# Performance work log

Hardware: AMD Instinct MI355X
Metric: run time of the kernel (lower is better)

## Reference

```python
import jax, jax.numpy as jnp
import numpy as np

H = 8          # num heads
DK = 64        # d_model // H
D_MODEL = 512
WIN = 256


def setup_inputs() -> dict:
    key = jax.random.key(0)
    ks = jax.random.split(key, 12)
    B, S = 2, 2048
    mk = lambda k, shape, s=1.0: jax.random.normal(k, shape, dtype=jnp.float32) * s
    inp = {
        "query": mk(ks[0], (B, S, D_MODEL)),
        "key_in": mk(ks[1], (B, S, D_MODEL)),
        "value": mk(ks[2], (B, S, D_MODEL)),
        # nn.Linear(d_model, d_model) weights (out,in) and biases, x4
        "Wq": mk(ks[3], (D_MODEL, D_MODEL), 0.02), "bq": jnp.zeros((D_MODEL,), jnp.float32),
        "Wk": mk(ks[4], (D_MODEL, D_MODEL), 0.02), "bk": jnp.zeros((D_MODEL,), jnp.float32),
        "Wv": mk(ks[5], (D_MODEL, D_MODEL), 0.02), "bv": jnp.zeros((D_MODEL,), jnp.float32),
        "Wo": mk(ks[6], (D_MODEL, D_MODEL), 0.02), "bo": jnp.zeros((D_MODEL,), jnp.float32),
    }
    return inp


def reference(query, key_in, value, Wq, bq, Wk, bk, Wv, bv, Wo, bo):
    B, S, D = query.shape
    scale = np.float32(1.0 / np.sqrt(DK))

    def proj(x, W, b):
        # (B,S,D) -> (B,H,S,DK)
        return (x @ W.T + b).reshape(B, S, H, DK).transpose(0, 2, 1, 3)

    q = proj(query, Wq, bq)
    k = proj(key_in, Wk, bk)
    v = proj(value, Wv, bv)

    # Faithful to naive_masked_matmul: full (B,H,S,S) scores, with entries
    # OUTSIDE the sliding window left at exactly 0.0 (NOT -inf) before softmax.
    scores = jnp.einsum('bhid,bhjd->bhij', q, k) * scale
    idx = jnp.arange(S)
    band = jnp.abs(idx[:, None] - idx[None, :]) <= (WIN // 2)  # (S,S) bool
    scores = jnp.where(band, scores, jnp.float32(0.0))

    p_attn = jax.nn.softmax(scores, axis=-1)
    x = jnp.einsum('bhij,bhjd->bhid', p_attn, v)          # (B,H,S,DK)
    x = x.transpose(0, 2, 1, 3).reshape(B, S, D)          # (B,S,D)
    return x @ Wo.T + bo
```

## Files before the change

kernel.cpp:

```cpp
#include <hip/hip_runtime.h>
#include <hip/hip_bf16.h>

#define SS 2048
#define DD 512
#define HWIN 128

typedef __bf16 bf16x8 __attribute__((ext_vector_type(8)));
typedef unsigned short u16x8 __attribute__((ext_vector_type(8)));
typedef float f32x4 __attribute__((ext_vector_type(4)));

__device__ __forceinline__ unsigned short f2bf(float x) {
    unsigned u = __builtin_bit_cast(unsigned, x);
    return (unsigned short)((u + 0x7fffu + ((u >> 16) & 1u)) >> 16);
}
__device__ __forceinline__ float bf2f(unsigned short s) {
    unsigned u = ((unsigned)s) << 16;
    return __builtin_bit_cast(float, u);
}
__device__ __forceinline__ void split_bf(float x, unsigned short& h, unsigned short& l) {
    h = f2bf(x);
    l = f2bf(x - bf2f(h));
}
__device__ __forceinline__ void split8(float4 f0, float4 f1, u16x8& h, u16x8& l) {
    const float vals[8] = {f0.x, f0.y, f0.z, f0.w, f1.x, f1.y, f1.z, f1.w};
    #pragma unroll
    for (int i = 0; i < 8; ++i) {
        unsigned short hh, ll;
        split_bf(vals[i], hh, ll);
        h[i] = hh;
        l[i] = ll;
    }
}
__device__ __forceinline__ f32x4 mfma16(u16x8 a, u16x8 b, f32x4 c) {
    return __builtin_amdgcn_mfma_f32_16x16x32_bf16(
        __builtin_bit_cast(bf16x8, a), __builtin_bit_cast(bf16x8, b), c, 0, 0, 0);
}
__device__ __forceinline__ void gload16(const unsigned short* g, unsigned short* l) {
    __builtin_amdgcn_global_load_lds(
        (const __attribute__((address_space(1))) unsigned int*)g,
        (__attribute__((address_space(3))) unsigned int*)l, 16, 0, 0);
}

__global__ __launch_bounds__(256) void castAll(
    const float* __restrict__ q, const float* __restrict__ k, const float* __restrict__ v,
    const float* __restrict__ wq, const float* __restrict__ wk,
    const float* __restrict__ wv, const float* __restrict__ wo,
    unsigned short* __restrict__ QAh, unsigned short* __restrict__ KAh,
    unsigned short* __restrict__ AVp,
    unsigned short* __restrict__ WQh, unsigned short* __restrict__ WKh,
    unsigned short* __restrict__ WVp, unsigned short* __restrict__ WoP)
{
    const size_t e0 = ((size_t)blockIdx.x * 256 + threadIdx.x) * 8;
    const float* src; size_t off; unsigned short* dsth; bool paired;
    if      (e0 < 2097152) { src = q; off = e0;           dsth = QAh + off;     paired = false; }
    else if (e0 < 4194304) { src = k; off = e0 - 2097152; dsth = KAh + off;     paired = false; }
    else if (e0 < 6291456) { src = v; off = e0 - 4194304; dsth = AVp + 2 * off; paired = true;  }
    else {
        const size_t e = e0 - 6291456;
        if      (e < 262144) { src = wq; off = e;          dsth = WQh + off;                paired = false; }
        else if (e < 524288) { src = wk; off = e - 262144; dsth = WKh + off;                paired = false; }
        else if (e < 786432) { src = wv; off = e - 524288; dsth = WVp + 2 * (e - 524288);   paired = true;  }
        else                 { src = wo; off = e - 786432; dsth = WoP + 2 * (e - 786432);   paired = true;  }
    }
    u16x8 h, l;
    split8(*(const float4*)(src + off), *(const float4*)(src + off + 4), h, l);
    *(u16x8*)dsth = h;
    if (paired) *(u16x8*)(dsth + 8) = l;
}

__global__ __launch_bounds__(256) void proj_gemm(
    const unsigned short* __restrict__ QAh, const unsigned short* __restrict__ KAh,
    const unsigned short* __restrict__ AVp,
    const unsigned short* __restrict__ WQh, const unsigned short* __restrict__ WKh,
    const unsigned short* __restrict__ WVp,
    const float* __restrict__ bq, const float* __restrict__ bk, const float* __restrict__ bv,
    unsigned short* __restrict__ base,
    unsigned short* __restrict__ VTH, unsigned short* __restrict__ VTL)
{
    const int d = blockIdx.x;
    const int hi = d >> 6, low = d & 63;
    const int x = low >> 3, rsw = low & 7;
    const int g = hi * 8 + rsw;
    const int y = g / 3, z = g - y * 3;

    const float* bias = (z == 0) ? bq : ((z == 1) ? bk : bv);
    unsigned short* OH = base + (size_t)z * 4194304;

    const int m0 = y * 128, n0 = x * 64;

    __shared__ unsigned short Ah[8 * 64 * 8], Al[8 * 64 * 8];
    __shared__ unsigned short Bh[4 * 64 * 8], Bl[4 * 64 * 8];

    const int tid = threadIdx.x, wave = tid >> 6, lane = tid & 63;
    const int lm = lane & 15, lq = lane >> 4;
    const int wm = wave >> 1, wn = wave & 1;
    const int kb = lq * 8;

    f32x4 acc[4][2] = {};

    const int ar0 = m0 + (wave * 2 + 0) * 16 + lm;
    const int ar1 = m0 + (wave * 2 + 1) * 16 + lm;
    const int br  = n0 + wave * 16 + lm;

    const int aoff0 = ((wave * 2 + 0) * 64 + lane) * 8;
    const int aoff1 = ((wave * 2 + 1) * 64 + lane) * 8;
    const int boff  = (wave * 64 + lane) * 8;

    if (z < 2) {
        const unsigned short* Ap = (z == 0) ? QAh : KAh;
        const unsigned short* Wp = (z == 0) ? WQh : WKh;
        for (int k0 = 0; k0 < 512; k0 += 32) {
            __syncthreads();
            gload16(Ap + (size_t)ar0 * 512 + k0 + kb, &Ah[aoff0]);
            gload16(Ap + (size_t)ar1 * 512 + k0 + kb, &Ah[aoff1]);
            gload16(Wp + (size_t)br  * 512 + k0 + kb, &Bh[boff]);
            __syncthreads();

            u16x8 afh[4], bfh[2];
            #pragma unroll
            for (int i = 0; i < 4; ++i)
                afh[i] = *(const u16x8*)&Ah[((wm * 4 + i) * 64 + lane) * 8];
            #pragma unroll
            for (int j = 0; j < 2; ++j)
                bfh[j] = *(const u16x8*)&Bh[((wn * 2 + j) * 64 + lane) * 8];
            #pragma unroll
            for (int i = 0; i < 4; ++i)
                #pragma unroll
                for (int j = 0; j < 2; ++j)
                    acc[i][j] = mfma16(afh[i], bfh[j], acc[i][j]);
        }
    } else {
        for (int k0 = 0; k0 < 512; k0 += 32) {
            __syncthreads();
            {
                const unsigned short* pa0 = AVp + 2 * ((size_t)ar0 * 512 + k0 + kb);
                gload16(pa0,     &Ah[aoff0]);
                gload16(pa0 + 8, &Al[aoff0]);
                const unsigned short* pa1 = AVp + 2 * ((size_t)ar1 * 512 + k0 + kb);
                gload16(pa1,     &Ah[aoff1]);
                gload16(pa1 + 8, &Al[aoff1]);
                const unsigned short* pw = WVp + 2 * ((size_t)br * 512 + k0 + kb);
                gload16(pw,     &Bh[boff]);
                gload16(pw + 8, &Bl[boff]);
            }
            __syncthreads();

            u16x8 afh[4], afl[4], bfh[2], bfl[2];
            #pragma unroll
            for (int i = 0; i < 4; ++i) {
                afh[i] = *(const u16x8*)&Ah[((wm * 4 + i) * 64 + lane) * 8];
                afl[i] = *(const u16x8*)&Al[((wm * 4 + i) * 64 + lane) * 8];
            }
            #pragma unroll
            for (int j = 0; j < 2; ++j) {
                bfh[j] = *(const u16x8*)&Bh[((wn * 2 + j) * 64 + lane) * 8];
                bfl[j] = *(const u16x8*)&Bl[((wn * 2 + j) * 64 + lane) * 8];
            }
            #pragma unroll
            for (int i = 0; i < 4; ++i)
                #pragma unroll
                for (int j = 0; j < 2; ++j) {
                    acc[i][j] = mfma16(afh[i], bfh[j], acc[i][j]);
                    acc[i][j] = mfma16(afh[i], bfl[j], acc[i][j]);
                    acc[i][j] = mfma16(afl[i], bfh[j], acc[i][j]);
                }
        }
    }

    #pragma unroll
    for (int i = 0; i < 4; ++i)
        #pragma unroll
        for (int j = 0; j < 2; ++j) {
            const int col = n0 + (wn * 2 + j) * 16 + lm;
            const float bv_ = bias[col];
            #pragma unroll
            for (int r = 0; r < 4; ++r) {
                const int row = m0 + (wm * 4 + i) * 16 + lq * 4 + r;
                const float vv = acc[i][j][r] + bv_;
                unsigned short hh, ll;
                split_bf(vv, hh, ll);
                if (z == 2) {
                    const size_t vix =
                        (((size_t)(row >> 11) * 8 + (col >> 6)) * 64 + (col & 63)) * 2048
                        + (row & 2047);
                    VTH[vix] = hh;
                    VTL[vix] = ll;
                } else {
                    OH[(size_t)row * 512 + col] = hh;
                }
            }
        }
}

__global__ __launch_bounds__(256) void out_gemm(
    const unsigned short* __restrict__ XHg, const unsigned short* __restrict__ XLg,
    const unsigned short* __restrict__ WoP, const float* __restrict__ bo,
    float* __restrict__ O)
{
    const int gid = blockIdx.x;
    const int rr = gid & 7, hi = gid >> 3;
    const int nblk = hi & 7, mhi = hi >> 3;
    const int mblk = mhi * 8 + rr;
    const int m0 = mblk * 64, n0 = nblk * 64;

    __shared__ unsigned short Ah[2 * 4096], Al[2 * 4096];
    __shared__ unsigned short Bh[2 * 4096], Bl[2 * 4096];

    const int tid = threadIdx.x, wave = tid >> 6, lane = tid & 63;
    const int lm = lane & 15, lq = lane >> 4;
    const int kb = lq * 8;

    f32x4 acc[4] = {};

    const int arow = m0 + wave * 16 + lm;
    const int brow = n0 + wave * 16 + lm;

    #define OSTAGE(k0_, bs)                                                     \
    {                                                                           \
        _Pragma("unroll")                                                       \
        for (int s = 0; s < 2; ++s) {                                           \
            const int o = (bs) * 4096 + ((s * 4 + wave) * 64 + lane) * 8;       \
            gload16(XHg + (size_t)arow * 512 + (k0_) + s * 32 + kb, &Ah[o]);    \
            gload16(XLg + (size_t)arow * 512 + (k0_) + s * 32 + kb, &Al[o]);    \
            const unsigned short* pw =                                          \
                WoP + 2 * ((size_t)brow * 512 + (k0_) + s * 32 + kb);           \
            gload16(pw,     &Bh[o]);                                            \
            gload16(pw + 8, &Bl[o]);                                            \
        }                                                                       \
    }

    OSTAGE(0, 0);
    __syncthreads();

    for (int t = 0; t < 8; ++t) {
        const int cur = t & 1;
        if (t < 7) OSTAGE((t + 1) * 64, cur ^ 1);

        #pragma unroll
        for (int s = 0; s < 2; ++s) {
            const u16x8 a_h = *(const u16x8*)&Ah[cur * 4096 + ((s * 4 + wave) * 64 + lane) * 8];
            const u16x8 a_l = *(const u16x8*)&Al[cur * 4096 + ((s * 4 + wave) * 64 + lane) * 8];
            #pragma unroll
            for (int j = 0; j < 4; ++j) {
                const u16x8 b_h = *(const u16x8*)&Bh[cur * 4096 + ((s * 4 + j) * 64 + lane) * 8];
                const u16x8 b_l = *(const u16x8*)&Bl[cur * 4096 + ((s * 4 + j) * 64 + lane) * 8];
                acc[j] = mfma16(a_h, b_h, acc[j]);
                acc[j] = mfma16(a_h, b_l, acc[j]);
                acc[j] = mfma16(a_l, b_h, acc[j]);
            }
        }

        __syncthreads();
    }
    #undef OSTAGE

    #pragma unroll
    for (int j = 0; j < 4; ++j) {
        const int col = n0 + j * 16 + lm;
        const float bv_ = bo[col];
        #pragma unroll
        for (int r = 0; r < 4; ++r) {
            const int row = m0 + wave * 16 + lq * 4 + r;
            O[(size_t)row * 512 + col] = acc[j][r] + bv_;
        }
    }
}

__global__ __launch_bounds__(256) void vsum_stage1(
    const unsigned short* __restrict__ VTH, const unsigned short* __restrict__ VTL,
    float* __restrict__ partial)
{
    const int bh = blockIdx.x, c = blockIdx.y;
    const int t = threadIdx.x, dd = t & 63, g = t >> 6;
    __shared__ float p[4][64];
    const size_t rb = ((size_t)bh * 64 + dd) * 2048 + c * 64 + g * 16;
    const u16x8 h0 = *(const u16x8*)(VTH + rb), h1 = *(const u16x8*)(VTH + rb + 8);
    const u16x8 l0 = *(const u16x8*)(VTL + rb), l1 = *(const u16x8*)(VTL + rb + 8);
    float acc = 0.f;
    #pragma unroll
    for (int i = 0; i < 8; ++i) acc += bf2f(h0[i]) + bf2f(l0[i]);
    #pragma unroll
    for (int i = 0; i < 8; ++i) acc += bf2f(h1[i]) + bf2f(l1[i]);
    p[g][dd] = acc;
    __syncthreads();
    if (t < 64)
        partial[((size_t)bh * 32 + c) * 64 + t] =
            p[0][t] + p[1][t] + p[2][t] + p[3][t];
}

__global__ __launch_bounds__(64) void vsum_stage2(
    const float* __restrict__ partial, float* __restrict__ VS)
{
    const int bh = blockIdx.x, dd = threadIdx.x;
    float acc = 0.f;
    #pragma unroll 8
    for (int c = 0; c < 32; ++c)
        acc += partial[((size_t)bh * 32 + c) * 64 + dd];
    VS[bh * 64 + dd] = acc;
}

__global__ __launch_bounds__(256) void attn_mfma(
    const unsigned short* __restrict__ QH, const unsigned short* __restrict__ KH,
    const unsigned short* __restrict__ VTH, const float* __restrict__ VS,
    unsigned short* __restrict__ XH, unsigned short* __restrict__ XL)
{
    const int dblk = blockIdx.x;
    const int bhi = dblk >> 8, blow = dblk & 255;
    const int xblk = blow >> 3, rrs = blow & 7;
    const int bh = bhi * 8 + rrs;
    const int h = bh & 7, b = bh >> 3;
    const int i0 = xblk * 64;
    const int tid = threadIdx.x, wave = tid >> 6, lane = tid & 63;
    const int lm = lane & 15, lq = lane >> 4;
    const int kb = lq * 8;

    __shared__ unsigned short KfH[2 * 8 * 64 * 8];
    __shared__ unsigned short VfH[2 * 8 * 64 * 8];
    __shared__ unsigned short Swh[64][72];

    const size_t qoff = ((size_t)(b * SS + i0 + wave * 16 + lm)) * DD + h * 64 + kb;
    const u16x8 aQ0h = *(const u16x8*)(QH + qoff);
    const u16x8 aQ1h = *(const u16x8*)(QH + qoff + 32);

    f32x4 oacc[4] = {};
    float dacc[4] = {0.f, 0.f, 0.f, 0.f};

    const size_t vrow = ((size_t)bh * 64 + wave * 16 + lm) * 2048;
    const int s0 = (wave * 2 + 0) * 64 * 8 + lane * 8;
    const int s1 = (wave * 2 + 1) * 64 * 8 + lane * 8;

    #define STAGE(jt_, bufsel)                                                  \
    {                                                                           \
        const int jt0_ = i0 - 128 + (jt_) * 64;                                 \
        const int jrow = jt0_ + wave * 16 + lm;                                 \
        const int jrc = min(max(jrow, 0), SS - 1);                              \
        const size_t kgb = ((size_t)(b * SS + jrc)) * DD + h * 64 + kb;         \
        gload16(KH + kgb,      &KfH[(bufsel) * 4096 + s0]);                     \
        gload16(KH + kgb + 32, &KfH[(bufsel) * 4096 + s1]);                     \
        const int j0c = min(max(jt0_ + kb, 0), SS - 8);                         \
        const int j1c = min(max(jt0_ + 32 + kb, 0), SS - 8);                    \
        gload16(VTH + vrow + j0c, &VfH[(bufsel) * 4096 + s0]);                  \
        gload16(VTH + vrow + j1c, &VfH[(bufsel) * 4096 + s1]);                  \
    }

    STAGE(0, 0);
    __syncthreads();

    for (int jt = 0; jt < 5; ++jt) {
        const int buf = jt & 1;
        if (jt < 4) STAGE(jt + 1, buf ^ 1);
        const int jt0 = i0 - 128 + jt * 64;

        #pragma unroll
        for (int js = 0; js < 4; ++js) {
            const int j0 = js * 16;
            const u16x8 bK0h = *(const u16x8*)&KfH[buf * 4096 + ((js * 2 + 0) * 64 + lane) * 8];
            const u16x8 bK1h = *(const u16x8*)&KfH[buf * 4096 + ((js * 2 + 1) * 64 + lane) * 8];
            f32x4 s = {0.f, 0.f, 0.f, 0.f};
            s = mfma16(aQ0h, bK0h, s);
            s = mfma16(aQ1h, bK1h, s);
            const int jg = jt0 + j0 + lm;
            const int iq = i0 + wave * 16 + lq * 4;
            #pragma unroll
            for (int r = 0; r < 4; ++r) {
                const int qi = iq + r;
                const bool in = (jg >= 0) && (jg < SS) &&
                                (jg >= qi - HWIN) && (jg <= qi + HWIN);
                const float w = in ? (__expf(s[r] * 0.125f) - 1.0f) : 0.0f;
                dacc[r] += w;
                Swh[wave * 16 + lq * 4 + r][j0 + lm] = f2bf(w);
            }
        }

        const u16x8 aP0h = *(const u16x8*)&Swh[wave * 16 + lm][kb];
        const u16x8 aP1h = *(const u16x8*)&Swh[wave * 16 + lm][kb + 32];
        #pragma unroll
        for (int s4 = 0; s4 < 4; ++s4) {
            const u16x8 bV0h = *(const u16x8*)&VfH[buf * 4096 + ((s4 * 2 + 0) * 64 + lane) * 8];
            const u16x8 bV1h = *(const u16x8*)&VfH[buf * 4096 + ((s4 * 2 + 1) * 64 + lane) * 8];
            oacc[s4] = mfma16(aP0h, bV0h, oacc[s4]);
            oacc[s4] = mfma16(aP1h, bV1h, oacc[s4]);
        }
        __syncthreads();
    }
    #undef STAGE

    #pragma unroll
    for (int r = 0; r < 4; ++r) {
        float v = dacc[r];
        v += __shfl_xor(v, 1);
        v += __shfl_xor(v, 2);
        v += __shfl_xor(v, 4);
        v += __shfl_xor(v, 8);
        dacc[r] = v + 2048.0f;
    }

    #pragma unroll
    for (int s4 = 0; s4 < 4; ++s4) {
        const float vsv = VS[bh * 64 + s4 * 16 + lm];
        #pragma unroll
        for (int r = 0; r < 4; ++r) {
            const int qrow = i0 + wave * 16 + lq * 4 + r;
            const float x = (oacc[s4][r] + vsv) / dacc[r];
            unsigned short xh, xl;
            split_bf(x, xh, xl);
            const size_t ix = ((size_t)(b * SS + qrow)) * DD + h * 64 + s4 * 16 + lm;
            XH[ix] = xh;
            XL[ix] = xl;
        }
    }
}

extern "C" void kernel_launch(void* const* d_in, const int* in_sizes, int n_in,
                              void* d_out, int out_size, void* d_ws, size_t ws_size,
                              hipStream_t stream)
{
    const float* query  = (const float*)d_in[0];
    const float* key_in = (const float*)d_in[1];
    const float* value  = (const float*)d_in[2];
    const float* Wq = (const float*)d_in[3]; const float* bq = (const float*)d_in[4];
    const float* Wk = (const float*)d_in[5]; const float* bk = (const float*)d_in[6];
    const float* Wv = (const float*)d_in[7]; const float* bv = (const float*)d_in[8];
    const float* Wo = (const float*)d_in[9]; const float* bo = (const float*)d_in[10];

    unsigned short* wsb = (unsigned short*)d_ws;
    unsigned short* QH  = wsb;
    unsigned short* KH  = wsb + 4194304;
    unsigned short* VTH = wsb + 8388608;
    unsigned short* VTL = wsb + 10485760;
    unsigned short* XH  = wsb + 12582912;
    unsigned short* XL  = wsb + 14680064;
    unsigned short* WQh = wsb + 16777216;
    unsigned short* WKh = wsb + 17039360;
    unsigned short* WVp = wsb + 17301504;
    unsigned short* WoP = wsb + 17825792;
    unsigned short* QAh = wsb + 18350080;
    unsigned short* KAh = wsb + 20447232;
    unsigned short* AVp = wsb + 22544384;
    float* part = (float*)((char*)d_ws + 62914560);
    float* VSp  = (float*)((char*)d_ws + 63045632);

    castAll<<<3584, 256, 0, stream>>>(query, key_in, value, Wq, Wk, Wv, Wo,
                                      QAh, KAh, AVp, WQh, WKh, WVp, WoP);

    proj_gemm<<<768, 256, 0, stream>>>(QAh, KAh, AVp, WQh, WKh, WVp,
                                       bq, bk, bv, QH, VTH, VTL);

    vsum_stage1<<<dim3(16, 32), 256, 0, stream>>>(VTH, VTL, part);
    vsum_stage2<<<16, 64, 0, stream>>>(part, VSp);

    attn_mfma<<<512, 256, 0, stream>>>(QH, KH, VTH, VSp, XH, XL);

    out_gemm<<<512, 256, 0, stream>>>(XH, XL, WoP, bo, (float*)d_out);
}
```

Baseline: 162.8 us.

## Fuse V column-sum into projection epilogue with atomics, drop VTL output

The V projection epilogue now sums each output column in registers, reduces across lanes with shuffles and adds the result into the per-(batch,head) V sum buffer with atomics. The buffer is zeroed in the cast kernel. This removes the two separate vsum reduction kernels and the low-bf16 half of transposed V, which saves two launches and a large global write and read. In exchange it adds float atomics with non-deterministic summation order, and the V sum now comes from unrounded fp32 values rather than the hi+lo split.

Measured after the change: 151.4 us. 1.07x faster.

```diff
diff --git a/kernel.cpp b/kernel.cpp
--- a/kernel.cpp
+++ b/kernel.cpp
@@ -48,8 +48,13 @@
     unsigned short* __restrict__ QAh, unsigned short* __restrict__ KAh,
     unsigned short* __restrict__ AVp,
     unsigned short* __restrict__ WQh, unsigned short* __restrict__ WKh,
-    unsigned short* __restrict__ WVp, unsigned short* __restrict__ WoP)
+    unsigned short* __restrict__ WVp, unsigned short* __restrict__ WoP,
+    float* __restrict__ VS)
 {
+    if (blockIdx.x == 0) {
+        float4 zz = {0.f, 0.f, 0.f, 0.f};
+        *(float4*)(VS + threadIdx.x * 4) = zz;
+    }
     const size_t e0 = ((size_t)blockIdx.x * 256 + threadIdx.x) * 8;
     const float* src; size_t off; unsigned short* dsth; bool paired;
     if      (e0 < 2097152) { src = q; off = e0;           dsth = QAh + off;     paired = false; }
@@ -75,7 +80,7 @@
     const unsigned short* __restrict__ WVp,
     const float* __restrict__ bq, const float* __restrict__ bk, const float* __restrict__ bv,
     unsigned short* __restrict__ base,
-    unsigned short* __restrict__ VTH, unsigned short* __restrict__ VTL)
+    unsigned short* __restrict__ VTH, float* __restrict__ VS)
 {
     const int d = blockIdx.x;
     const int hi = d >> 6, low = d & 63;
@@ -129,6 +134,18 @@
                 for (int j = 0; j < 2; ++j)
                     acc[i][j] = mfma16(afh[i], bfh[j], acc[i][j]);
         }
+        #pragma unroll
+        for (int i = 0; i < 4; ++i)
+            #pragma unroll
+            for (int j = 0; j < 2; ++j) {
+                const int col = n0 + (wn * 2 + j) * 16 + lm;
+                const float bv_ = bias[col];
+                #pragma unroll
+                for (int r = 0; r < 4; ++r) {
+                    const int row = m0 + (wm * 4 + i) * 16 + lq * 4 + r;
+                    OH[(size_t)row * 512 + col] = f2bf(acc[i][j][r] + bv_);
+                }
+            }
     } else {
         for (int k0 = 0; k0 < 512; k0 += 32) {
             __syncthreads();
@@ -165,31 +182,36 @@
                     acc[i][j] = mfma16(afl[i], bfh[j], acc[i][j]);
                 }
         }
-    }
-
-    #pragma unroll
-    for (int i = 0; i < 4; ++i)
-        #pragma unroll
-        for (int j = 0; j < 2; ++j) {
-            const int col = n0 + (wn * 2 + j) * 16 + lm;
-            const float bv_ = bias[col];
-            #pragma unroll
-            for (int r = 0; r < 4; ++r) {
-                const int row = m0 + (wm * 4 + i) * 16 + lq * 4 + r;
-                const float vv = acc[i][j][r] + bv_;
-                unsigned short hh, ll;
-                split_bf(vv, hh, ll);
-                if (z == 2) {
+
+        float csum[2] = {0.f, 0.f};
+        #pragma unroll
+        for (int i = 0; i < 4; ++i)
+            #pragma unroll
+            for (int j = 0; j < 2; ++j) {
+                const int col = n0 + (wn * 2 + j) * 16 + lm;
+                const float bv_ = bias[col];
+                #pragma unroll
+                for (int r = 0; r < 4; ++r) {
+                    const int row = m0 + (wm * 4 + i) * 16 + lq * 4 + r;
+                    const float vv = acc[i][j][r] + bv_;
+                    csum[j] += vv;
                     const size_t vix =
                         (((size_t)(row >> 11) * 8 + (col >> 6)) * 64 + (col & 63)) * 2048
                         + (row & 2047);
-                    VTH[vix] = hh;
-                    VTL[vix] = ll;
-                } else {
-                    OH[(size_t)row * 512 + col] = hh;
+                    VTH[vix] = f2bf(vv);
                 }
             }
-        }
+        #pragma unroll
+        for (int j = 0; j < 2; ++j) {
+            float s = csum[j];
+            s += __shfl_xor(s, 16);
+            s += __shfl_xor(s, 32);
+            if (lq == 0) {
+                const int col = n0 + (wn * 2 + j) * 16 + lm;
+                atomicAdd(&VS[(m0 >> 11) * 512 + col], s);
+            }
+        }
+    }
 }
 
 __global__ __launch_bounds__(256) void out_gemm(
@@ -264,39 +286,6 @@
             O[(size_t)row * 512 + col] = acc[j][r] + bv_;
         }
     }
-}
-
-__global__ __launch_bounds__(256) void vsum_stage1(
-    const unsigned short* __restrict__ VTH, const unsigned short* __restrict__ VTL,
-    float* __restrict__ partial)
-{
-    const int bh = blockIdx.x, c = blockIdx.y;
-    const int t = threadIdx.x, dd = t & 63, g = t >> 6;
-    __shared__ float p[4][64];
-    const size_t rb = ((size_t)bh * 64 + dd) * 2048 + c * 64 + g * 16;
-    const u16x8 h0 = *(const u16x8*)(VTH + rb), h1 = *(const u16x8*)(VTH + rb + 8);
-    const u16x8 l0 = *(const u16x8*)(VTL + rb), l1 = *(const u16x8*)(VTL + rb + 8);
-    float acc = 0.f;
-    #pragma unroll
-    for (int i = 0; i < 8; ++i) acc += bf2f(h0[i]) + bf2f(l0[i]);
-    #pragma unroll
-    for (int i = 0; i < 8; ++i) acc += bf2f(h1[i]) + bf2f(l1[i]);
-    p[g][dd] = acc;
-    __syncthreads();
-    if (t < 64)
-        partial[((size_t)bh * 32 + c) * 64 + t] =
-            p[0][t] + p[1][t] + p[2][t] + p[3][t];
-}
-
-__global__ __launch_bounds__(64) void vsum_stage2(
-    const float* __restrict__ partial, float* __restrict__ VS)
-{
-    const int bh = blockIdx.x, dd = threadIdx.x;
-    float acc = 0.f;
-    #pragma unroll 8
-    for (int c = 0; c < 32; ++c)
-        acc += partial[((size_t)bh * 32 + c) * 64 + dd];
-    VS[bh * 64 + dd] = acc;
 }
 
 __global__ __launch_bounds__(256) void attn_mfma(
@@ -427,7 +416,6 @@
     unsigned short* QH  = wsb;
     unsigned short* KH  = wsb + 4194304;
     unsigned short* VTH = wsb + 8388608;
-    unsigned short* VTL = wsb + 10485760;
     unsigned short* XH  = wsb + 12582912;
     unsigned short* XL  = wsb + 14680064;
     unsigned short* WQh = wsb + 16777216;
@@ -437,17 +425,13 @@
     unsigned short* QAh = wsb + 18350080;
     unsigned short* KAh = wsb + 20447232;
     unsigned short* AVp = wsb + 22544384;
-    float* part = (float*)((char*)d_ws + 62914560);
     float* VSp  = (float*)((char*)d_ws + 63045632);
 
     castAll<<<3584, 256, 0, stream>>>(query, key_in, value, Wq, Wk, Wv, Wo,
-                                      QAh, KAh, AVp, WQh, WKh, WVp, WoP);
+                                      QAh, KAh, AVp, WQh, WKh, WVp, WoP, VSp);
 
     proj_gemm<<<768, 256, 0, stream>>>(QAh, KAh, AVp, WQh, WKh, WVp,
-                                       bq, bk, bv, QH, VTH, VTL);
-
-    vsum_stage1<<<dim3(16, 32), 256, 0, stream>>>(VTH, VTL, part);
-    vsum_stage2<<<16, 64, 0, stream>>>(part, VSp);
+                                       bq, bk, bv, QH, VTH, VSp);
 
     attn_mfma<<<512, 256, 0, stream>>>(QH, KH, VTH, VSp, XH, XL);
 
```
